# Kernel tuning notes

Measured on AMD Instinct MI355X. Metric: run time of the kernel, lower is better.

Reference implementation:

```python
import jax, jax.numpy as jnp
import numpy as np

N = 50000
E = 800000
IN_CH = 128
HID = 32
HEADS = 4
OUT_CH = 32
NEG_SLOPE = 0.2


def setup_inputs() -> dict:
    key = jax.random.key(0)
    ks = jax.random.split(key, 12)
    x = jax.random.normal(ks[0], (N, IN_CH), dtype=jnp.float32)
    edge_index = jax.random.randint(ks[1], (2, E), 0, N, dtype=jnp.int64)
    s1 = 1.0 / np.sqrt(IN_CH)
    s2 = 1.0 / np.sqrt(HEADS * HID)
    W1 = jax.random.normal(ks[2], (IN_CH, HEADS * HID), dtype=jnp.float32) * s1
    att_src1 = jax.random.normal(ks[3], (HEADS, HID), dtype=jnp.float32) * s2
    att_dst1 = jax.random.normal(ks[4], (HEADS, HID), dtype=jnp.float32) * s2
    b1 = jnp.zeros((HEADS * HID,), dtype=jnp.float32)
    W2 = jax.random.normal(ks[5], (HEADS * HID, OUT_CH), dtype=jnp.float32) * s2
    att_src2 = jax.random.normal(ks[6], (1, OUT_CH), dtype=jnp.float32) * (1.0 / np.sqrt(OUT_CH))
    att_dst2 = jax.random.normal(ks[7], (1, OUT_CH), dtype=jnp.float32) * (1.0 / np.sqrt(OUT_CH))
    b2 = jnp.zeros((OUT_CH,), dtype=jnp.float32)
    return {"x": x, "edge_index": edge_index, "W1": W1, "att_src1": att_src1,
            "att_dst1": att_dst1, "b1": b1, "W2": W2, "att_src2": att_src2,
            "att_dst2": att_dst2, "b2": b2}


def _gat_layer(x, src, dst, W, att_src, att_dst, bias, heads, out_ch, concat):
    n = x.shape[0]
    xw = (x @ W).reshape(n, heads, out_ch)            # [N,H,C]
    a_src = jnp.einsum('nhc,hc->nh', xw, att_src)     # [N,H]
    a_dst = jnp.einsum('nhc,hc->nh', xw, att_dst)
    e = a_src[src] + a_dst[dst]                        # [E,H]
    e = jnp.where(e > 0, e, NEG_SLOPE * e)             # LeakyReLU(0.2)
    # edge-softmax grouped by destination node (stable)
    e_max = jax.ops.segment_max(e, dst, num_segments=n)
    e_max = jnp.where(jnp.isfinite(e_max), e_max, 0.0)
    e_exp = jnp.exp(e - e_max[dst])
    denom = jax.ops.segment_sum(e_exp, dst, num_segments=n)
    alpha = e_exp / (denom[dst] + 1e-16)               # [E,H]
    msg = xw[src] * alpha[:, :, None]                  # [E,H,C]
    out = jax.ops.segment_sum(msg, dst, num_segments=n)  # [N,H,C]
    if concat:
        out = out.reshape(n, heads * out_ch)
    else:
        out = out.mean(axis=1)
    return out + bias


def reference(x, edge_index, W1, att_src1, att_dst1, b1, W2, att_src2, att_dst2, b2):
    # PyG GATConv adds self-loops by default
    loops = jnp.arange(N, dtype=edge_index.dtype)
    src = jnp.concatenate([edge_index[0], loops])
    dst = jnp.concatenate([edge_index[1], loops])
    h = _gat_layer(x, src, dst, W1, att_src1, att_dst1, b1, HEADS, HID, True)
    h = jax.nn.elu(h)
    # dropout p=0.5 is identity at inference (training=False)
    out = _gat_layer(h, src, dst, W2, att_src2, att_dst2, b2, 1, OUT_CH, False)
    return out
```

## Files before the change

### kernel.cpp

```cpp
#include <hip/hip_runtime.h>
#include <hip/hip_fp16.h>

#define N_NODES 50000
#define E_EDGES 800000
#define ETOT (E_EDGES + N_NODES)
#define IN_CH 128
#define HH 128
#define HEADS 4
#define HID 32
#define OUT_CH 32
#define NEG 0.2f

#define GEMM_BLOCKS ((N_NODES + 127) / 128)
#define FILL_BLOCKS ((ETOT + 1023) / 1024)
#define XP 132

__global__ __launch_bounds__(256, 2) void gemm1_fused(const float* __restrict__ x,
                                                      const float* __restrict__ W1,
                                                      const float* __restrict__ att_s,
                                                      const float* __restrict__ att_d,
                                                      const int* __restrict__ ei,
                                                      __half* __restrict__ xwh,
                                                      float* __restrict__ a1s,
                                                      float* __restrict__ a1d,
                                                      int* __restrict__ deg,
                                                      int* __restrict__ idx) {
    __shared__ float Xs[32][XP];
    __shared__ float Ws[32][XP];
    int t = threadIdx.x;

    if (blockIdx.x >= GEMM_BLOCKS) {
        int base = (blockIdx.x - GEMM_BLOCKS) * 1024 + t;
#pragma unroll
        for (int q = 0; q < 4; ++q) {
            int e = base + q * 256;
            if (e < ETOT) {
                int d = (e < E_EDGES) ? ei[E_EDGES + e] : e - E_EDGES;
                idx[e] = atomicAdd(deg + d, 1);
            }
        }
        return;
    }

    int tx = t & 15, ty = t >> 4;
    int row0 = blockIdx.x * 128;
    float acc[8][8] = {};

    for (int k0 = 0; k0 < IN_CH; k0 += 32) {
#pragma unroll
        for (int p = 0; p < 4; ++p) {
            int i2 = t + p * 256;
            int kk = i2 >> 5, c4 = i2 & 31;
            float4 v = *(const float4*)&W1[(size_t)(k0 + kk) * HH + c4 * 4];
            *(float4*)&Ws[kk][c4 * 4] = v;
        }
#pragma unroll
        for (int p = 0; p < 4; ++p) {
            int i2 = t + p * 256;
            int rr = i2 >> 3, c4 = i2 & 7;
            int row = row0 + rr;
            float4 v = make_float4(0.f, 0.f, 0.f, 0.f);
            if (row < N_NODES) v = *(const float4*)&x[(size_t)row * IN_CH + k0 + c4 * 4];
            Xs[c4 * 4 + 0][rr] = v.x;
            Xs[c4 * 4 + 1][rr] = v.y;
            Xs[c4 * 4 + 2][rr] = v.z;
            Xs[c4 * 4 + 3][rr] = v.w;
        }
        __syncthreads();
#pragma unroll 8
        for (int kk = 0; kk < 32; ++kk) {
            float4 xa0 = *(const float4*)&Xs[kk][ty * 4];
            float4 xa1 = *(const float4*)&Xs[kk][ty * 4 + 64];
            float4 wb0 = *(const float4*)&Ws[kk][tx * 4];
            float4 wb1 = *(const float4*)&Ws[kk][tx * 4 + 64];
            float xa[8] = {xa0.x, xa0.y, xa0.z, xa0.w, xa1.x, xa1.y, xa1.z, xa1.w};
            float wb[8] = {wb0.x, wb0.y, wb0.z, wb0.w, wb1.x, wb1.y, wb1.z, wb1.w};
#pragma unroll
            for (int i = 0; i < 8; ++i)
#pragma unroll
                for (int j = 0; j < 8; ++j)
                    acc[i][j] = fmaf(xa[i], wb[j], acc[i][j]);
        }
        __syncthreads();
    }

    float asr[8], adr[8];
#pragma unroll
    for (int j = 0; j < 8; ++j) {
        int col = tx * 4 + (j & 3) + ((j >> 2) << 6);
        asr[j] = att_s[col];
        adr[j] = att_d[col];
    }
    int hA = tx >> 3;

#pragma unroll
    for (int i = 0; i < 8; ++i) {
        int row = row0 + ty * 4 + (i < 4 ? i : 60 + i);
        if (row < N_NODES) {
            union { __half2 h2; unsigned u; } c0, c1, c2, c3;
            c0.h2 = __floats2half2_rn(acc[i][0], acc[i][1]);
            c1.h2 = __floats2half2_rn(acc[i][2], acc[i][3]);
            c2.h2 = __floats2half2_rn(acc[i][4], acc[i][5]);
            c3.h2 = __floats2half2_rn(acc[i][6], acc[i][7]);
            *(uint2*)&xwh[(size_t)row * HH + tx * 4]      = make_uint2(c0.u, c1.u);
            *(uint2*)&xwh[(size_t)row * HH + tx * 4 + 64] = make_uint2(c2.u, c3.u);
        }
        float psA = 0.f, pdA = 0.f, psB = 0.f, pdB = 0.f;
#pragma unroll
        for (int j = 0; j < 4; ++j) {
            psA = fmaf(acc[i][j], asr[j], psA);
            pdA = fmaf(acc[i][j], adr[j], pdA);
            psB = fmaf(acc[i][j + 4], asr[j + 4], psB);
            pdB = fmaf(acc[i][j + 4], adr[j + 4], pdB);
        }
#pragma unroll
        for (int off = 1; off < 8; off <<= 1) {
            psA += __shfl_xor(psA, off, 16);
            pdA += __shfl_xor(pdA, off, 16);
            psB += __shfl_xor(psB, off, 16);
            pdB += __shfl_xor(pdB, off, 16);
        }
        if ((tx & 7) == 0 && row < N_NODES) {
            a1s[row * 4 + hA]     = psA;
            a1d[row * 4 + hA]     = pdA;
            a1s[row * 4 + hA + 2] = psB;
            a1d[row * 4 + hA + 2] = pdB;
        }
    }
}

__device__ __forceinline__ int block_incl_scan(int v, int t) {
    for (int off = 1; off < 64; off <<= 1) {
        int n = __shfl_up(v, off, 64);
        if ((t & 63) >= off) v += n;
    }
    __shared__ int wsum[4];
    if ((t & 63) == 63) wsum[t >> 6] = v;
    __syncthreads();
    int w = t >> 6;
    if (w > 0) {
        int add = 0;
        for (int k = 0; k < w; ++k) add += wsum[k];
        v += add;
    }
    __syncthreads();
    return v;
}

#define NCHUNK ((N_NODES + 255) / 256)

__global__ void scan_s1(const int* __restrict__ deg, int* __restrict__ rowptr,
                        int* __restrict__ partials) {
    int t = threadIdx.x;
    int i = blockIdx.x * 256 + t;
    int v = (i < N_NODES) ? deg[i] : 0;
    int s = block_incl_scan(v, t);
    if (i < N_NODES) rowptr[i + 1] = s;
    if (t == 255) partials[blockIdx.x] = s;
}

__global__ void scan_s2(int* __restrict__ partials) {
    int t = threadIdx.x;
    int v = (t < NCHUNK) ? partials[t] : 0;
    int s = block_incl_scan(v, t);
    if (t < NCHUNK) partials[t] = s;
}

__global__ void scan_s3(int* __restrict__ rowptr, const int* __restrict__ partials) {
    int i = blockIdx.x * blockDim.x + threadIdx.x;
    if (i == 0) rowptr[0] = 0;
    if (i < N_NODES) {
        int c = i >> 8;
        if (c > 0) rowptr[i + 1] += partials[c - 1];
    }
}

__global__ void place_csr(const int* __restrict__ ei, const int* __restrict__ idx,
                          const int* __restrict__ rowptr, int* __restrict__ csr_src) {
    int e = blockIdx.x * blockDim.x + threadIdx.x;
    if (e >= ETOT) return;
    int s, d;
    if (e < E_EDGES) { s = ei[e]; d = ei[E_EDGES + e]; }
    else { s = e - E_EDGES; d = s; }
    csr_src[rowptr[d] + idx[e]] = s;
}

__global__ void gather1_g2(const int* __restrict__ rowptr, const int* __restrict__ csr_src,
                           const float* __restrict__ a1s, const float* __restrict__ a1d,
                           const __half* __restrict__ xwh,
                           const float* __restrict__ b1, const float* __restrict__ W2,
                           const float* __restrict__ att_s2, const float* __restrict__ att_d2,
                           __half* __restrict__ hw2h,
                           float* __restrict__ a2s, float* __restrict__ a2d) {
    __shared__ float Wl[HH * OUT_CH];
    __shared__ float hs[4][HH];
    int t = threadIdx.x;
    for (int i = t; i < HH * OUT_CH; i += 256) Wl[i] = W2[i];
    __syncthreads();

    int wid = t >> 6;
    int d = blockIdx.x * 4 + wid;
    int l = t & 63;
    int h = l >> 4;
    float ad = a1d[d * 4 + h];
    int p0 = rowptr[d], p1 = rowptr[d + 1];
    float acc0 = 0.f, acc1 = 0.f, wsum = 0.f;
    int p = p0;
    for (; p + 3 < p1; p += 4) {
        int s0 = csr_src[p], s1 = csr_src[p + 1], s2 = csr_src[p + 2], s3 = csr_src[p + 3];
        float v0 = a1s[s0 * 4 + h] + ad; v0 = v0 > 0.f ? v0 : NEG * v0;
        float v1 = a1s[s1 * 4 + h] + ad; v1 = v1 > 0.f ? v1 : NEG * v1;
        float v2 = a1s[s2 * 4 + h] + ad; v2 = v2 > 0.f ? v2 : NEG * v2;
        float v3 = a1s[s3 * 4 + h] + ad; v3 = v3 > 0.f ? v3 : NEG * v3;
        float w0 = __expf(v0), w1 = __expf(v1), w2 = __expf(v2), w3 = __expf(v3);
        float2 f0 = __half22float2(*(const __half2*)&xwh[(size_t)s0 * HH + 2 * l]);
        float2 f1 = __half22float2(*(const __half2*)&xwh[(size_t)s1 * HH + 2 * l]);
        float2 f2 = __half22float2(*(const __half2*)&xwh[(size_t)s2 * HH + 2 * l]);
        float2 f3 = __half22float2(*(const __half2*)&xwh[(size_t)s3 * HH + 2 * l]);
        acc0 = fmaf(w0, f0.x, acc0); acc1 = fmaf(w0, f0.y, acc1);
        acc0 = fmaf(w1, f1.x, acc0); acc1 = fmaf(w1, f1.y, acc1);
        acc0 = fmaf(w2, f2.x, acc0); acc1 = fmaf(w2, f2.y, acc1);
        acc0 = fmaf(w3, f3.x, acc0); acc1 = fmaf(w3, f3.y, acc1);
        wsum += (w0 + w1) + (w2 + w3);
    }
    for (; p < p1; ++p) {
        int s = csr_src[p];
        float v = a1s[s * 4 + h] + ad; v = v > 0.f ? v : NEG * v;
        float w = __expf(v);
        float2 f = __half22float2(*(const __half2*)&xwh[(size_t)s * HH + 2 * l]);
        acc0 = fmaf(w, f.x, acc0); acc1 = fmaf(w, f.y, acc1);
        wsum += w;
    }
    float r = 1.f / (wsum + 1e-16f);
    float2 bv = *(const float2*)&b1[2 * l];
    float h0 = acc0 * r + bv.x;
    float h1 = acc1 * r + bv.y;
    h0 = h0 > 0.f ? h0 : (__expf(h0) - 1.f);
    h1 = h1 > 0.f ? h1 : (__expf(h1) - 1.f);
    *(float2*)&hs[wid][2 * l] = make_float2(h0, h1);

    int o = l & 31, half = l >> 5;
    const float* hrow = &hs[wid][half * 64];
    const float* wcol = &Wl[half * 64 * OUT_CH + o];
    float acc = 0.f;
#pragma unroll 8
    for (int j = 0; j < 64; ++j) acc = fmaf(hrow[j], wcol[j * OUT_CH], acc);
    acc += __shfl_xor(acc, 32, 64);

    if (half == 0) hw2h[(size_t)d * OUT_CH + o] = __float2half_rn(acc);

    float ps = acc * att_s2[o], pd = acc * att_d2[o];
#pragma unroll
    for (int off = 16; off; off >>= 1) {
        ps += __shfl_xor(ps, off, 32);
        pd += __shfl_xor(pd, off, 32);
    }
    if (l == 0) { a2s[d] = ps; a2d[d] = pd; }
}

__global__ void gather2(const int* __restrict__ rowptr, const int* __restrict__ csr_src,
                        const float* __restrict__ a2s, const float* __restrict__ a2d,
                        const __half* __restrict__ hw2h, const float* __restrict__ b2,
                        float* __restrict__ out) {
    int t = threadIdx.x;
    int d = blockIdx.x * 8 + (t >> 5);
    if (d >= N_NODES) return;
    int o = t & 31;
    float ad = a2d[d];
    int p0 = rowptr[d], p1 = rowptr[d + 1];
    float acc = 0.f, wsum = 0.f;
    int p = p0;
    for (; p + 3 < p1; p += 4) {
        int s0 = csr_src[p], s1 = csr_src[p + 1], s2 = csr_src[p + 2], s3 = csr_src[p + 3];
        float v0 = a2s[s0] + ad; v0 = v0 > 0.f ? v0 : NEG * v0;
        float v1 = a2s[s1] + ad; v1 = v1 > 0.f ? v1 : NEG * v1;
        float v2 = a2s[s2] + ad; v2 = v2 > 0.f ? v2 : NEG * v2;
        float v3 = a2s[s3] + ad; v3 = v3 > 0.f ? v3 : NEG * v3;
        float w0 = __expf(v0), w1 = __expf(v1), w2 = __expf(v2), w3 = __expf(v3);
        float x0 = __half2float(hw2h[(size_t)s0 * OUT_CH + o]);
        float x1 = __half2float(hw2h[(size_t)s1 * OUT_CH + o]);
        float x2 = __half2float(hw2h[(size_t)s2 * OUT_CH + o]);
        float x3 = __half2float(hw2h[(size_t)s3 * OUT_CH + o]);
        acc = fmaf(w0, x0, acc); acc = fmaf(w1, x1, acc);
        acc = fmaf(w2, x2, acc); acc = fmaf(w3, x3, acc);
        wsum += (w0 + w1) + (w2 + w3);
    }
    for (; p < p1; ++p) {
        int s = csr_src[p];
        float v = a2s[s] + ad; v = v > 0.f ? v : NEG * v;
        float w = __expf(v);
        acc = fmaf(w, __half2float(hw2h[(size_t)s * OUT_CH + o]), acc);
        wsum += w;
    }
    out[(size_t)d * OUT_CH + o] = acc / (wsum + 1e-16f) + b2[o];
}

extern "C" void kernel_launch(void* const* d_in, const int* in_sizes, int n_in,
                              void* d_out, int out_size, void* d_ws, size_t ws_size,
                              hipStream_t stream) {
    const float* x   = (const float*)d_in[0];
    const int*   ei  = (const int*)d_in[1];
    const float* W1  = (const float*)d_in[2];
    const float* as1 = (const float*)d_in[3];
    const float* ad1 = (const float*)d_in[4];
    const float* b1  = (const float*)d_in[5];
    const float* W2  = (const float*)d_in[6];
    const float* as2 = (const float*)d_in[7];
    const float* ad2 = (const float*)d_in[8];
    const float* b2  = (const float*)d_in[9];
    float* out = (float*)d_out;
    float* ws  = (float*)d_ws;

    __half* xwh   = (__half*)ws;
    __half* hw2h  = (__half*)(ws + 3200000);
    float* a1s    = ws + 4000000;
    float* a1d    = ws + 4200000;
    float* a2s    = ws + 4400000;
    float* a2d    = ws + 4450000;
    int*   deg    = (int*)(ws + 4500000);
    int*   rowptr = (int*)(ws + 4550000);
    int*   parts  = (int*)(ws + 4600016);
    int*   csr_src= (int*)(ws + 4600272);
    int*   idx    = (int*)(ws + 5450272);

    hipMemsetAsync(deg, 0, (size_t)N_NODES * sizeof(int), stream);

    gemm1_fused<<<GEMM_BLOCKS + FILL_BLOCKS, 256, 0, stream>>>(
        x, W1, as1, ad1, ei, xwh, a1s, a1d, deg, idx);

    scan_s1  <<<NCHUNK, 256, 0, stream>>>(deg, rowptr, parts);
    scan_s2  <<<1, 256, 0, stream>>>(parts);
    scan_s3  <<<(N_NODES + 255) / 256, 256, 0, stream>>>(rowptr, parts);
    place_csr<<<(ETOT + 255) / 256, 256, 0, stream>>>(ei, idx, rowptr, csr_src);

    gather1_g2<<<N_NODES / 4, 256, 0, stream>>>(rowptr, csr_src, a1s, a1d, xwh,
                                                b1, W2, as2, ad2, hw2h, a2s, a2d);

    gather2  <<<(N_NODES + 7) / 8, 256, 0, stream>>>(rowptr, csr_src, a2s, a2d, hw2h, b2, out);
}
```

Measured before the change: 172.8 us.

## Precompute layer-1 edge weights during CSR placement into 32-byte edge records

The CSR placement kernel now computes the four per-head LeakyReLU+exp attention weights for each edge and writes them with the source index into a 32-byte record per edge. The layer-1 gather then reads the source and its head's weight from the record instead of gathering a1s per edge and recomputing exp, and its main loop is unrolled by eight. This removes the scattered a1s loads and redundant exp work from the gather, at the cost of writing and reading 32 bytes per edge instead of 4. gather2 also reads source indices from these records at a 32-byte stride, which wastes bandwidth there.

```diff
diff --git a/kernel.cpp b/kernel.cpp
--- a/kernel.cpp
+++ b/kernel.cpp
@@ -175,18 +175,30 @@
     }
 }
 
-__global__ void place_csr(const int* __restrict__ ei, const int* __restrict__ idx,
-                          const int* __restrict__ rowptr, int* __restrict__ csr_src) {
+__global__ void place_csr_w(const int* __restrict__ ei, const int* __restrict__ idx,
+                            const int* __restrict__ rowptr,
+                            const float* __restrict__ a1s, const float* __restrict__ a1d,
+                            float* __restrict__ edge32) {
     int e = blockIdx.x * blockDim.x + threadIdx.x;
     if (e >= ETOT) return;
     int s, d;
     if (e < E_EDGES) { s = ei[e]; d = ei[E_EDGES + e]; }
     else { s = e - E_EDGES; d = s; }
-    csr_src[rowptr[d] + idx[e]] = s;
-}
-
-__global__ void gather1_g2(const int* __restrict__ rowptr, const int* __restrict__ csr_src,
-                           const float* __restrict__ a1s, const float* __restrict__ a1d,
+    int pos = rowptr[d] + idx[e];
+    float4 as = *(const float4*)&a1s[s * 4];
+    float4 ad = *(const float4*)&a1d[d * 4];
+    float4 w; float v;
+    v = as.x + ad.x; v = v > 0.f ? v : NEG * v; w.x = __expf(v);
+    v = as.y + ad.y; v = v > 0.f ? v : NEG * v; w.y = __expf(v);
+    v = as.z + ad.z; v = v > 0.f ? v : NEG * v; w.z = __expf(v);
+    v = as.w + ad.w; v = v > 0.f ? v : NEG * v; w.w = __expf(v);
+    float* rec = edge32 + (size_t)pos * 8;
+    *(uint4*)rec         = make_uint4((unsigned)s, 0u, 0u, 0u);
+    *(float4*)(rec + 4)  = w;
+}
+
+__global__ void gather1_g2(const int* __restrict__ rowptr,
+                           const float* __restrict__ edge32,
                            const __half* __restrict__ xwh,
                            const float* __restrict__ b1, const float* __restrict__ W2,
                            const float* __restrict__ att_s2, const float* __restrict__ att_d2,
@@ -202,31 +214,23 @@
     int d = blockIdx.x * 4 + wid;
     int l = t & 63;
     int h = l >> 4;
-    float ad = a1d[d * 4 + h];
+    const int* ei32 = (const int*)edge32;
     int p0 = rowptr[d], p1 = rowptr[d + 1];
     float acc0 = 0.f, acc1 = 0.f, wsum = 0.f;
     int p = p0;
-    for (; p + 3 < p1; p += 4) {
-        int s0 = csr_src[p], s1 = csr_src[p + 1], s2 = csr_src[p + 2], s3 = csr_src[p + 3];
-        float v0 = a1s[s0 * 4 + h] + ad; v0 = v0 > 0.f ? v0 : NEG * v0;
-        float v1 = a1s[s1 * 4 + h] + ad; v1 = v1 > 0.f ? v1 : NEG * v1;
-        float v2 = a1s[s2 * 4 + h] + ad; v2 = v2 > 0.f ? v2 : NEG * v2;
-        float v3 = a1s[s3 * 4 + h] + ad; v3 = v3 > 0.f ? v3 : NEG * v3;
-        float w0 = __expf(v0), w1 = __expf(v1), w2 = __expf(v2), w3 = __expf(v3);
-        float2 f0 = __half22float2(*(const __half2*)&xwh[(size_t)s0 * HH + 2 * l]);
-        float2 f1 = __half22float2(*(const __half2*)&xwh[(size_t)s1 * HH + 2 * l]);
-        float2 f2 = __half22float2(*(const __half2*)&xwh[(size_t)s2 * HH + 2 * l]);
-        float2 f3 = __half22float2(*(const __half2*)&xwh[(size_t)s3 * HH + 2 * l]);
-        acc0 = fmaf(w0, f0.x, acc0); acc1 = fmaf(w0, f0.y, acc1);
-        acc0 = fmaf(w1, f1.x, acc0); acc1 = fmaf(w1, f1.y, acc1);
-        acc0 = fmaf(w2, f2.x, acc0); acc1 = fmaf(w2, f2.y, acc1);
-        acc0 = fmaf(w3, f3.x, acc0); acc1 = fmaf(w3, f3.y, acc1);
-        wsum += (w0 + w1) + (w2 + w3);
+    for (; p + 7 < p1; p += 8) {
+#define LD(k) int s##k = ei32[(size_t)(p + k) * 8]; \
+              float w##k = edge32[(size_t)(p + k) * 8 + 4 + h];
+        LD(0) LD(1) LD(2) LD(3) LD(4) LD(5) LD(6) LD(7)
+#undef LD
+#define FM(k) { float2 f = __half22float2(*(const __half2*)&xwh[(size_t)s##k * HH + 2 * l]); \
+                acc0 = fmaf(w##k, f.x, acc0); acc1 = fmaf(w##k, f.y, acc1); wsum += w##k; }
+        FM(0) FM(1) FM(2) FM(3) FM(4) FM(5) FM(6) FM(7)
+#undef FM
     }
     for (; p < p1; ++p) {
-        int s = csr_src[p];
-        float v = a1s[s * 4 + h] + ad; v = v > 0.f ? v : NEG * v;
-        float w = __expf(v);
+        int s = ei32[(size_t)p * 8];
+        float w = edge32[(size_t)p * 8 + 4 + h];
         float2 f = __half22float2(*(const __half2*)&xwh[(size_t)s * HH + 2 * l]);
         acc0 = fmaf(w, f.x, acc0); acc1 = fmaf(w, f.y, acc1);
         wsum += w;
@@ -258,7 +262,7 @@
     if (l == 0) { a2s[d] = ps; a2d[d] = pd; }
 }
 
-__global__ void gather2(const int* __restrict__ rowptr, const int* __restrict__ csr_src,
+__global__ void gather2(const int* __restrict__ rowptr, const float* __restrict__ edge32,
                         const float* __restrict__ a2s, const float* __restrict__ a2d,
                         const __half* __restrict__ hw2h, const float* __restrict__ b2,
                         float* __restrict__ out) {
@@ -266,12 +270,16 @@
     int d = blockIdx.x * 8 + (t >> 5);
     if (d >= N_NODES) return;
     int o = t & 31;
+    const int* ei32 = (const int*)edge32;
     float ad = a2d[d];
     int p0 = rowptr[d], p1 = rowptr[d + 1];
     float acc = 0.f, wsum = 0.f;
     int p = p0;
     for (; p + 3 < p1; p += 4) {
-        int s0 = csr_src[p], s1 = csr_src[p + 1], s2 = csr_src[p + 2], s3 = csr_src[p + 3];
+        int s0 = ei32[(size_t)(p + 0) * 8];
+        int s1 = ei32[(size_t)(p + 1) * 8];
+        int s2 = ei32[(size_t)(p + 2) * 8];
+        int s3 = ei32[(size_t)(p + 3) * 8];
         float v0 = a2s[s0] + ad; v0 = v0 > 0.f ? v0 : NEG * v0;
         float v1 = a2s[s1] + ad; v1 = v1 > 0.f ? v1 : NEG * v1;
         float v2 = a2s[s2] + ad; v2 = v2 > 0.f ? v2 : NEG * v2;
@@ -286,7 +294,7 @@
         wsum += (w0 + w1) + (w2 + w3);
     }
     for (; p < p1; ++p) {
-        int s = csr_src[p];
+        int s = ei32[(size_t)p * 8];
         float v = a2s[s] + ad; v = v > 0.f ? v : NEG * v;
         float w = __expf(v);
         acc = fmaf(w, __half2float(hw2h[(size_t)s * OUT_CH + o]), acc);
@@ -320,8 +328,8 @@
     int*   deg    = (int*)(ws + 4500000);
     int*   rowptr = (int*)(ws + 4550000);
     int*   parts  = (int*)(ws + 4600016);
-    int*   csr_src= (int*)(ws + 4600272);
-    int*   idx    = (int*)(ws + 5450272);
+    int*   idx    = (int*)(ws + 4600272);
+    float* edge32 = ws + 5450272;
 
     hipMemsetAsync(deg, 0, (size_t)N_NODES * sizeof(int), stream);
 
@@ -331,10 +339,10 @@
     scan_s1  <<<NCHUNK, 256, 0, stream>>>(deg, rowptr, parts);
     scan_s2  <<<1, 256, 0, stream>>>(parts);
     scan_s3  <<<(N_NODES + 255) / 256, 256, 0, stream>>>(rowptr, parts);
-    place_csr<<<(ETOT + 255) / 256, 256, 0, stream>>>(ei, idx, rowptr, csr_src);
-
-    gather1_g2<<<N_NODES / 4, 256, 0, stream>>>(rowptr, csr_src, a1s, a1d, xwh,
+    place_csr_w<<<(ETOT + 255) / 256, 256, 0, stream>>>(ei, idx, rowptr, a1s, a1d, edge32);
+
+    gather1_g2<<<N_NODES / 4, 256, 0, stream>>>(rowptr, edge32, xwh,
                                                 b1, W2, as2, ad2, hw2h, a2s, a2d);
 
-    gather2  <<<(N_NODES + 7) / 8, 256, 0, stream>>>(rowptr, csr_src, a2s, a2d, hw2h, b2, out);
-}
+    gather2  <<<(N_NODES + 7) / 8, 256, 0, stream>>>(rowptr, edge32, a2s, a2d, hw2h, b2, out);
+}
```

Result: slower. 193.6 us (+12.0%).

## Use 32 lanes per node in layer-1 gather with 4 channels per lane

Applied to the files above, without the earlier changes.

The layer-1 gather kernel now gives each destination node 32 lanes instead of a full 64-lane wavefront. Each lane loads four half-precision channels with one 8-byte load and keeps four accumulators, so a block handles 8 nodes and the grid is halved. The fused layer-2 projection now does the whole 128-long dot product per lane, which removes the cross-half shuffle. The aim is to halve the redundant per-edge index, attention-score and exp work per node and to widen the memory loads. In exchange, each lane carries a longer serial FMA chain and two nodes share one wavefront, which may diverge when their degrees differ.

```diff
diff --git a/kernel.cpp b/kernel.cpp
--- a/kernel.cpp
+++ b/kernel.cpp
@@ -193,18 +193,19 @@
                            __half* __restrict__ hw2h,
                            float* __restrict__ a2s, float* __restrict__ a2d) {
     __shared__ float Wl[HH * OUT_CH];
-    __shared__ float hs[4][HH];
+    __shared__ float hs[8][HH];
     int t = threadIdx.x;
     for (int i = t; i < HH * OUT_CH; i += 256) Wl[i] = W2[i];
     __syncthreads();
 
-    int wid = t >> 6;
-    int d = blockIdx.x * 4 + wid;
-    int l = t & 63;
-    int h = l >> 4;
+    int wid = t >> 5;
+    int d = blockIdx.x * 8 + wid;
+    int l = t & 31;
+    int h = l >> 3;
     float ad = a1d[d * 4 + h];
     int p0 = rowptr[d], p1 = rowptr[d + 1];
-    float acc0 = 0.f, acc1 = 0.f, wsum = 0.f;
+    float acc0 = 0.f, acc1 = 0.f, acc2 = 0.f, acc3 = 0.f, wsum = 0.f;
+    union { float2 f2; __half2 h2[2]; } u0, u1, u2, u3;
     int p = p0;
     for (; p + 3 < p1; p += 4) {
         int s0 = csr_src[p], s1 = csr_src[p + 1], s2 = csr_src[p + 2], s3 = csr_src[p + 3];
@@ -213,43 +214,49 @@
         float v2 = a1s[s2 * 4 + h] + ad; v2 = v2 > 0.f ? v2 : NEG * v2;
         float v3 = a1s[s3 * 4 + h] + ad; v3 = v3 > 0.f ? v3 : NEG * v3;
         float w0 = __expf(v0), w1 = __expf(v1), w2 = __expf(v2), w3 = __expf(v3);
-        float2 f0 = __half22float2(*(const __half2*)&xwh[(size_t)s0 * HH + 2 * l]);
-        float2 f1 = __half22float2(*(const __half2*)&xwh[(size_t)s1 * HH + 2 * l]);
-        float2 f2 = __half22float2(*(const __half2*)&xwh[(size_t)s2 * HH + 2 * l]);
-        float2 f3 = __half22float2(*(const __half2*)&xwh[(size_t)s3 * HH + 2 * l]);
-        acc0 = fmaf(w0, f0.x, acc0); acc1 = fmaf(w0, f0.y, acc1);
-        acc0 = fmaf(w1, f1.x, acc0); acc1 = fmaf(w1, f1.y, acc1);
-        acc0 = fmaf(w2, f2.x, acc0); acc1 = fmaf(w2, f2.y, acc1);
-        acc0 = fmaf(w3, f3.x, acc0); acc1 = fmaf(w3, f3.y, acc1);
+        u0.f2 = *(const float2*)&xwh[(size_t)s0 * HH + 4 * l];
+        u1.f2 = *(const float2*)&xwh[(size_t)s1 * HH + 4 * l];
+        u2.f2 = *(const float2*)&xwh[(size_t)s2 * HH + 4 * l];
+        u3.f2 = *(const float2*)&xwh[(size_t)s3 * HH + 4 * l];
+#define FM(k, W) { float2 fa = __half22float2(u##k.h2[0]); float2 fb = __half22float2(u##k.h2[1]); \
+                   acc0 = fmaf(W, fa.x, acc0); acc1 = fmaf(W, fa.y, acc1); \
+                   acc2 = fmaf(W, fb.x, acc2); acc3 = fmaf(W, fb.y, acc3); }
+        FM(0, w0) FM(1, w1) FM(2, w2) FM(3, w3)
+#undef FM
         wsum += (w0 + w1) + (w2 + w3);
     }
     for (; p < p1; ++p) {
         int s = csr_src[p];
         float v = a1s[s * 4 + h] + ad; v = v > 0.f ? v : NEG * v;
         float w = __expf(v);
-        float2 f = __half22float2(*(const __half2*)&xwh[(size_t)s * HH + 2 * l]);
-        acc0 = fmaf(w, f.x, acc0); acc1 = fmaf(w, f.y, acc1);
+        u0.f2 = *(const float2*)&xwh[(size_t)s * HH + 4 * l];
+        float2 fa = __half22float2(u0.h2[0]);
+        float2 fb = __half22float2(u0.h2[1]);
+        acc0 = fmaf(w, fa.x, acc0); acc1 = fmaf(w, fa.y, acc1);
+        acc2 = fmaf(w, fb.x, acc2); acc3 = fmaf(w, fb.y, acc3);
         wsum += w;
     }
     float r = 1.f / (wsum + 1e-16f);
-    float2 bv = *(const float2*)&b1[2 * l];
+    float4 bv = *(const float4*)&b1[4 * l];
     float h0 = acc0 * r + bv.x;
     float h1 = acc1 * r + bv.y;
-    h0 = h0 > 0.f ? h0 : (__expf(h0) - 1.f);
-    h1 = h1 > 0.f ? h1 : (__expf(h1) - 1.f);
-    *(float2*)&hs[wid][2 * l] = make_float2(h0, h1);
-
-    int o = l & 31, half = l >> 5;
-    const float* hrow = &hs[wid][half * 64];
-    const float* wcol = &Wl[half * 64 * OUT_CH + o];
+    float h2v = acc2 * r + bv.z;
+    float h3v = acc3 * r + bv.w;
+    h0  = h0  > 0.f ? h0  : (__expf(h0)  - 1.f);
+    h1  = h1  > 0.f ? h1  : (__expf(h1)  - 1.f);
+    h2v = h2v > 0.f ? h2v : (__expf(h2v) - 1.f);
+    h3v = h3v > 0.f ? h3v : (__expf(h3v) - 1.f);
+    *(float4*)&hs[wid][4 * l] = make_float4(h0, h1, h2v, h3v);
+
+    const float* hrow = hs[wid];
+    const float* wcol = &Wl[l];
     float acc = 0.f;
 #pragma unroll 8
-    for (int j = 0; j < 64; ++j) acc = fmaf(hrow[j], wcol[j * OUT_CH], acc);
-    acc += __shfl_xor(acc, 32, 64);
-
-    if (half == 0) hw2h[(size_t)d * OUT_CH + o] = __float2half_rn(acc);
-
-    float ps = acc * att_s2[o], pd = acc * att_d2[o];
+    for (int j = 0; j < 128; ++j) acc = fmaf(hrow[j], wcol[j * OUT_CH], acc);
+
+    hw2h[(size_t)d * OUT_CH + l] = __float2half_rn(acc);
+
+    float ps = acc * att_s2[l], pd = acc * att_d2[l];
 #pragma unroll
     for (int off = 16; off; off >>= 1) {
         ps += __shfl_xor(ps, off, 32);
@@ -333,7 +340,7 @@
     scan_s3  <<<(N_NODES + 255) / 256, 256, 0, stream>>>(rowptr, parts);
     place_csr<<<(ETOT + 255) / 256, 256, 0, stream>>>(ei, idx, rowptr, csr_src);
 
-    gather1_g2<<<N_NODES / 4, 256, 0, stream>>>(rowptr, csr_src, a1s, a1d, xwh,
+    gather1_g2<<<N_NODES / 8, 256, 0, stream>>>(rowptr, csr_src, a1s, a1d, xwh,
                                                 b1, W2, as2, ad2, hw2h, a2s, a2d);
 
     gather2  <<<(N_NODES + 7) / 8, 256, 0, stream>>>(rowptr, csr_src, a2s, a2d, hw2h, b2, out);
```

After: 156.5 us (median of 2 runs). -9.4%, faster.
